# Optimization experiments

Hardware: AMD Instinct MI355X
Metric: run time of the kernel (lower is better)

Reference implementation:

```python
import jax, jax.numpy as jnp
import numpy as np

D = 256  # api_embed_channels
B = 8    # number of graphs
N = 128  # invoked APIs per graph (nodes); edges = N*N (fully connected incl. self-loops)
V = 10000


def setup_inputs() -> dict:
    key = jax.random.key(0)
    ks = jax.random.split(key, 12)
    s = 0.02
    return {
        "Xs": jax.random.normal(ks[0], (B, D), jnp.float32),
        "api_embeds": jax.random.normal(ks[1], (V, D), jnp.float32),
        "W1": jax.random.normal(ks[2], (2 * D, D), jnp.float32) * s,
        "b1": jnp.zeros((D,), jnp.float32),
        "W2": jax.random.normal(ks[3], (2 * D, D), jnp.float32) * s,
        "b2": jnp.zeros((D,), jnp.float32),
        "W3": jax.random.normal(ks[4], (2 * D, D), jnp.float32) * s,
        "b3": jnp.zeros((D,), jnp.float32),
        "W4": jax.random.normal(ks[5], (2 * D, 1), jnp.float32) * s,
        "b4": jnp.zeros((1,), jnp.float32),
        "invoked": jax.random.randint(ks[6], (B, N), 0, V, jnp.int32),
    }


def reference(Xs, api_embeds, W1, b1, W2, b2, W3, b3, W4, b4, invoked):
    # Gather invoked-API node features per graph: [B, N, D]
    feat = api_embeds[invoked]
    # Fully connected edge list in DGL insertion order: edge i -> (u=i//N, v=i%N).
    # src feats vary along axis 1 (u), dst feats along axis 2 (v).
    src = jnp.broadcast_to(feat[:, :, None, :], (B, N, N, D))
    dst = jnp.broadcast_to(feat[:, None, :, :], (B, N, N, D))
    # n2v_mlp1 per edge: Linear(2D -> D) on cat([src, dst])
    m = jnp.concatenate([src, dst], axis=-1) @ W1 + b1          # [B, N, N, D]
    # mean aggregation over incoming edges of dst v == mean over u (axis 1)
    e2n1 = jnp.mean(m, axis=1)                                   # [B, N, D]
    # n2n_mlp2: Linear(2D -> D) on cat([feat, e2n1])
    h = jnp.concatenate([feat, e2n1], axis=-1) @ W2 + b2         # [B, N, D]
    # n2v_mlp3 per edge: Linear(2D -> D) on cat([h_src, h_dst])
    hs = jnp.broadcast_to(h[:, :, None, :], (B, N, N, D))
    hd = jnp.broadcast_to(h[:, None, :, :], (B, N, N, D))
    ef = jnp.concatenate([hs, hd], axis=-1) @ W3 + b3            # [B, N, N, D]
    ef = ef.reshape(B, N * N, D)                                 # edge order u*N + v
    # edge_exist_mlp on cat([ef, x repeated per edge]): Linear(2D -> 1) + sigmoid
    x = jnp.broadcast_to(Xs[:, None, :], (B, N * N, D))
    logits = jnp.concatenate([ef, x], axis=-1) @ W4 + b4         # [B, N*N, 1]
    return jax.nn.sigmoid(logits)
```

## Files before the change

### kernel.cpp

```cpp
#include <hip/hip_runtime.h>


__device__ __forceinline__ float wred(float v) {
#pragma unroll
  for (int o = 32; o > 0; o >>= 1) v += __shfl_xor(v, o, 64);
  return v;
}
__device__ __forceinline__ float dot4(float4 a, float4 b) {
  return a.x * b.x + a.y * b.y + a.z * b.z + a.w * b.w;
}

#define OFF_PM   0
#define OFF_WA   131328
#define OFF_WB   131584
#define OFF_VA   131840
#define OFF_VB   132096
#define OFF_QS   132352
#define OFF_C0   132608
#define OFF_CALL 132616
#define OFF_FEAT 132624
#define WS_FLOATS_STAGED (OFF_FEAT + 262144)

__global__ __launch_bounds__(256) void k1(
    const float* __restrict__ Xs, const float* __restrict__ api,
    const float* __restrict__ W1, const float* __restrict__ b1,
    const float* __restrict__ W2, const float* __restrict__ b2,
    const float* __restrict__ W3, const float* __restrict__ b3,
    const float* __restrict__ W4, const float* __restrict__ b4,
    const int* __restrict__ invoked, float* __restrict__ ws) {
  const int blk = blockIdx.x, tid = threadIdx.x;
  float* PM = ws + OFF_PM;
  const float* W2bot = W2 + 256 * 256;
  __shared__ float w1s[2][256];
  __shared__ float4 part[2][4][64];

  if (blk < 256) {
    const int r0 = blk * 2;
    const int c4 = tid & 63, wv = tid >> 6;
    ((float*)w1s)[tid]       = W1[(size_t)r0 * 256 + tid];
    ((float*)w1s)[tid + 256] = W1[(size_t)r0 * 256 + 256 + tid];
    __syncthreads();
    const float4* w2b4 = (const float4*)W2bot;
    float4 a0 = make_float4(0.f, 0.f, 0.f, 0.f);
    float4 a1 = make_float4(0.f, 0.f, 0.f, 0.f);
    const int kb = wv * 64;
#pragma unroll 8
    for (int i = 0; i < 64; ++i) {
      int k = kb + i;
      float4 w = w2b4[k * 64 + c4];
      float x0 = w1s[0][k], x1 = w1s[1][k];
      a0.x += x0 * w.x; a0.y += x0 * w.y; a0.z += x0 * w.z; a0.w += x0 * w.w;
      a1.x += x1 * w.x; a1.y += x1 * w.y; a1.z += x1 * w.z; a1.w += x1 * w.w;
    }
    part[0][wv][c4] = a0;
    part[1][wv][c4] = a1;
    __syncthreads();
    if (tid < 128) {
      int row = tid >> 6, c = tid & 63;
      float4 p0 = part[row][0][c], p1 = part[row][1][c];
      float4 p2 = part[row][2][c], p3 = part[row][3][c];
      float4 s = make_float4(p0.x + p1.x + p2.x + p3.x,
                             p0.y + p1.y + p2.y + p3.y,
                             p0.z + p1.z + p2.z + p3.z,
                             p0.w + p1.w + p2.w + p3.w);
      int r = r0 + row;
      if (r >= 256) {
        float4 t = ((const float4*)(W2 + (size_t)(r - 256) * 256))[c];
        s.x += t.x; s.y += t.y; s.z += t.z; s.w += t.w;
      }
      ((float4*)(PM + (size_t)r * 256))[c] = s;
    }
  } else if (blk < 384) {
    const int lane = tid & 63, wv = tid >> 6;
    const int t = (blk - 256) * 4 + wv;
    float4 w4a = ((const float4*)W4)[lane];
    float4 rv = ((const float4*)(W3 + (size_t)t * 256))[lane];
    float s = wred(dot4(rv, w4a));
    if (lane == 0) {
      if (t < 256) ws[OFF_WA + t] = s; else ws[OFF_WB + t - 256] = s;
    }
  } else if (blk == 384) {
    const int lane = tid & 63, wv = tid >> 6;
    float4 w4a = ((const float4*)W4)[lane];
    float4 w4b4 = ((const float4*)W4)[lane + 64];
    float sb3 = wred(dot4(((const float4*)b3)[lane], w4a));
    for (int bi = wv; bi < 8; bi += 4) {
      float xd = wred(dot4(((const float4*)(Xs + (size_t)bi * 256))[lane], w4b4));
      if (lane == 0) ws[OFF_C0 + bi] = b4[0] + sb3 + xd;
    }
    const int c4 = tid & 63, rg = tid >> 6;
    const float4* w2b4 = (const float4*)W2bot;
    float4 acc = make_float4(0.f, 0.f, 0.f, 0.f);
#pragma unroll 8
    for (int i = 0; i < 64; ++i) {
      int k = rg * 64 + i;
      float4 w = w2b4[k * 64 + c4];
      float bv = b1[k];
      acc.x += bv * w.x; acc.y += bv * w.y; acc.z += bv * w.z; acc.w += bv * w.w;
    }
    part[0][rg][c4] = acc;
    __syncthreads();
    if (tid < 64) {
      float4 p0 = part[0][0][tid], p1 = part[0][1][tid];
      float4 p2 = part[0][2][tid], p3 = part[0][3][tid];
      float4 bb = ((const float4*)b2)[tid];
      float4 s = make_float4(p0.x + p1.x + p2.x + p3.x + bb.x,
                             p0.y + p1.y + p2.y + p3.y + bb.y,
                             p0.z + p1.z + p2.z + p3.z + bb.z,
                             p0.w + p1.w + p2.w + p3.w + bb.w);
      ((float4*)(PM + (size_t)512 * 256))[tid] = s;
    }
  } else {
    const int lane = tid & 63, wv = tid >> 6;
    const int row = (blk - 385) * 4 + wv;
    int idx = invoked[row];
    ((float4*)(ws + OFF_FEAT + (size_t)row * 256))[lane] =
        ((const float4*)(api + (size_t)idx * 256))[lane];
  }
}

__global__ __launch_bounds__(256) void k2(float* __restrict__ ws) {
  const int blk = blockIdx.x, tid = threadIdx.x;
  const int lane = tid & 63, wv = tid >> 6;
  const float* PM = ws + OFF_PM;
  float4 wa4 = ((const float4*)(ws + OFF_WA))[lane];
  float4 wb4 = ((const float4*)(ws + OFF_WB))[lane];
  if (blk < 128) {
    const int t = blk * 4 + wv;
    if (t < 256) {
      float4 rv = ((const float4*)(PM + (size_t)(256 + t) * 256))[lane];
      float sa = wred(dot4(rv, wa4));
      float sb = wred(dot4(rv, wb4));
      if (lane == 0) { ws[OFF_VA + t] = sa; ws[OFF_VB + t] = sb; }
    } else {
      float4 rv = ((const float4*)(PM + (size_t)(t - 256) * 256))[lane];
      float4 s4 = make_float4(wa4.x + wb4.x, wa4.y + wb4.y,
                              wa4.z + wb4.z, wa4.w + wb4.w);
      float s = wred(dot4(rv, s4));
      if (lane == 0) ws[OFF_QS + t - 256] = s;
    }
  } else {
    __shared__ float sAllSh;
    if (wv == 0) {
      float4 rv = ((const float4*)(PM + (size_t)512 * 256))[lane];
      float4 s4 = make_float4(wa4.x + wb4.x, wa4.y + wb4.y,
                              wa4.z + wb4.z, wa4.w + wb4.w);
      float s = wred(dot4(rv, s4));
      if (lane == 0) sAllSh = s;
    }
    __syncthreads();
    if (tid < 8) ws[OFF_CALL + tid] = ws[OFF_C0 + tid] + sAllSh;
  }
}

__global__ __launch_bounds__(1024) void k3(
    const float* __restrict__ api, const int* __restrict__ invoked,
    const float* __restrict__ ws, float* __restrict__ out, int staged) {
  const int g = blockIdx.x, tid = threadIdx.x;
  const int lane = tid & 63, wv = tid >> 6;
  __shared__ float Ash[128], Bsh[128], scsh[128];
  __shared__ float CbSh;

  float4 f[8];
  const int ub = wv * 8;
  if (staged) {
    const float4* fp =
        (const float4*)(ws + OFF_FEAT + (size_t)((g << 7) + ub) * 256);
#pragma unroll
    for (int i = 0; i < 8; ++i) f[i] = fp[(size_t)i * 64 + lane];
  } else {
    int idx[8];
#pragma unroll
    for (int i = 0; i < 8; ++i) idx[i] = invoked[(g << 7) + ub + i];
#pragma unroll
    for (int i = 0; i < 8; ++i)
      f[i] = ((const float4*)(api + (size_t)idx[i] * 256))[lane];
  }

  float4 va4 = ((const float4*)(ws + OFF_VA))[lane];
  float4 vb4 = ((const float4*)(ws + OFF_VB))[lane];
  float4 q4  = ((const float4*)(ws + OFF_QS))[lane];
#pragma unroll
  for (int i = 0; i < 8; ++i) {
    float sa = wred(dot4(f[i], va4));
    float sb = wred(dot4(f[i], vb4));
    float sc = wred(dot4(f[i], q4));
    if (lane == 0) { Ash[ub + i] = sa; Bsh[ub + i] = sb; scsh[ub + i] = sc; }
  }
  __syncthreads();
  if (wv == 0) {
    float t = scsh[lane] + scsh[lane + 64];
    t = wred(t);
    if (lane == 0) CbSh = t * (1.f / 128.f) + ws[OFF_CALL + g];
  }
  __syncthreads();
  const float Cb = CbSh;
  float4* ob = (float4*)(out + (g << 14));
#pragma unroll
  for (int j = 0; j < 4; ++j) {
    int e4 = tid + (j << 10);
    float a = Ash[e4 >> 5] + Cb;
    float4 bv = ((const float4*)Bsh)[e4 & 31];
    float4 r;
    r.x = 1.f / (1.f + __expf(-(a + bv.x)));
    r.y = 1.f / (1.f + __expf(-(a + bv.y)));
    r.z = 1.f / (1.f + __expf(-(a + bv.z)));
    r.w = 1.f / (1.f + __expf(-(a + bv.w)));
    ob[e4] = r;
  }
}

extern "C" void kernel_launch(void* const* d_in, const int* in_sizes, int n_in,
                              void* d_out, int out_size, void* d_ws, size_t ws_size,
                              hipStream_t stream) {
  const float* Xs  = (const float*)d_in[0];
  const float* api = (const float*)d_in[1];
  const float* W1  = (const float*)d_in[2];
  const float* b1  = (const float*)d_in[3];
  const float* W2  = (const float*)d_in[4];
  const float* b2  = (const float*)d_in[5];
  const float* W3  = (const float*)d_in[6];
  const float* b3  = (const float*)d_in[7];
  const float* W4  = (const float*)d_in[8];
  const float* b4  = (const float*)d_in[9];
  const int* invoked = (const int*)d_in[10];
  float* out = (float*)d_out;
  float* ws = (float*)d_ws;

  const int staged = (ws_size >= (size_t)WS_FLOATS_STAGED * sizeof(float));
  hipLaunchKernelGGL(k1, dim3(staged ? 641 : 385), dim3(256), 0, stream,
                     Xs, api, W1, b1, W2, b2, W3, b3, W4, b4, invoked, ws);
  hipLaunchKernelGGL(k2, dim3(129), dim3(256), 0, stream, ws);
  hipLaunchKernelGGL(k3, dim3(8), dim3(1024), 0, stream,
                     api, invoked, ws, out, staged);
}
```

Before: 25.98 us.

## Widen W1·W2 row tiles, drop feature staging, split k3 across 64 blocks

k1 now has each block compute 8 rows of the W1·W2 product instead of 2, so each W2 load is reused across more rows and the grid is smaller. The separate feature-gather blocks and their workspace staging are removed, and k3 always gathers embeddings directly. k3 launches 8 blocks per graph, each writing 16 rows of output, which spreads the output store and sigmoid across more CUs. The cost is that every block recomputes the same per-graph dot products, so the gather work is repeated 8 times. The wider tile also holds more accumulators per thread in k1, which raises register pressure.

Measured after the change: 22.91 us (median of 2 runs). 11.8% less time.

```diff
diff --git a/kernel.cpp b/kernel.cpp
--- a/kernel.cpp
+++ b/kernel.cpp
@@ -18,45 +18,50 @@
 #define OFF_QS   132352
 #define OFF_C0   132608
 #define OFF_CALL 132616
-#define OFF_FEAT 132624
-#define WS_FLOATS_STAGED (OFF_FEAT + 262144)
 
 __global__ __launch_bounds__(256) void k1(
-    const float* __restrict__ Xs, const float* __restrict__ api,
+    const float* __restrict__ Xs,
     const float* __restrict__ W1, const float* __restrict__ b1,
     const float* __restrict__ W2, const float* __restrict__ b2,
     const float* __restrict__ W3, const float* __restrict__ b3,
     const float* __restrict__ W4, const float* __restrict__ b4,
-    const int* __restrict__ invoked, float* __restrict__ ws) {
+    float* __restrict__ ws) {
   const int blk = blockIdx.x, tid = threadIdx.x;
   float* PM = ws + OFF_PM;
   const float* W2bot = W2 + 256 * 256;
-  __shared__ float w1s[2][256];
-  __shared__ float4 part[2][4][64];
-
-  if (blk < 256) {
-    const int r0 = blk * 2;
+  __shared__ float w1s[8][256];
+  __shared__ float4 part[8][4][64];
+
+  if (blk < 64) {
+    const int r0 = blk * 8;
     const int c4 = tid & 63, wv = tid >> 6;
-    ((float*)w1s)[tid]       = W1[(size_t)r0 * 256 + tid];
-    ((float*)w1s)[tid + 256] = W1[(size_t)r0 * 256 + 256 + tid];
+#pragma unroll
+    for (int i = 0; i < 8; ++i)
+      ((float*)w1s)[i * 256 + tid] = W1[(size_t)r0 * 256 + i * 256 + tid];
     __syncthreads();
     const float4* w2b4 = (const float4*)W2bot;
-    float4 a0 = make_float4(0.f, 0.f, 0.f, 0.f);
-    float4 a1 = make_float4(0.f, 0.f, 0.f, 0.f);
+    float4 acc[8];
+#pragma unroll
+    for (int i = 0; i < 8; ++i) acc[i] = make_float4(0.f, 0.f, 0.f, 0.f);
     const int kb = wv * 64;
-#pragma unroll 8
+#pragma unroll 4
     for (int i = 0; i < 64; ++i) {
       int k = kb + i;
       float4 w = w2b4[k * 64 + c4];
-      float x0 = w1s[0][k], x1 = w1s[1][k];
-      a0.x += x0 * w.x; a0.y += x0 * w.y; a0.z += x0 * w.z; a0.w += x0 * w.w;
-      a1.x += x1 * w.x; a1.y += x1 * w.y; a1.z += x1 * w.z; a1.w += x1 * w.w;
-    }
-    part[0][wv][c4] = a0;
-    part[1][wv][c4] = a1;
-    __syncthreads();
-    if (tid < 128) {
-      int row = tid >> 6, c = tid & 63;
+#pragma unroll
+      for (int r = 0; r < 8; ++r) {
+        float x = w1s[r][k];
+        acc[r].x += x * w.x; acc[r].y += x * w.y;
+        acc[r].z += x * w.z; acc[r].w += x * w.w;
+      }
+    }
+#pragma unroll
+    for (int r = 0; r < 8; ++r) part[r][wv][c4] = acc[r];
+    __syncthreads();
+#pragma unroll
+    for (int j = 0; j < 2; ++j) {
+      int item = tid + j * 256;
+      int row = item >> 6, c = item & 63;
       float4 p0 = part[row][0][c], p1 = part[row][1][c];
       float4 p2 = part[row][2][c], p3 = part[row][3][c];
       float4 s = make_float4(p0.x + p1.x + p2.x + p3.x,
@@ -70,16 +75,16 @@
       }
       ((float4*)(PM + (size_t)r * 256))[c] = s;
     }
-  } else if (blk < 384) {
+  } else if (blk < 192) {
     const int lane = tid & 63, wv = tid >> 6;
-    const int t = (blk - 256) * 4 + wv;
+    const int t = (blk - 64) * 4 + wv;
     float4 w4a = ((const float4*)W4)[lane];
     float4 rv = ((const float4*)(W3 + (size_t)t * 256))[lane];
     float s = wred(dot4(rv, w4a));
     if (lane == 0) {
       if (t < 256) ws[OFF_WA + t] = s; else ws[OFF_WB + t - 256] = s;
     }
-  } else if (blk == 384) {
+  } else {
     const int lane = tid & 63, wv = tid >> 6;
     float4 w4a = ((const float4*)W4)[lane];
     float4 w4b4 = ((const float4*)W4)[lane + 64];
@@ -110,12 +115,6 @@
                              p0.w + p1.w + p2.w + p3.w + bb.w);
       ((float4*)(PM + (size_t)512 * 256))[tid] = s;
     }
-  } else {
-    const int lane = tid & 63, wv = tid >> 6;
-    const int row = (blk - 385) * 4 + wv;
-    int idx = invoked[row];
-    ((float4*)(ws + OFF_FEAT + (size_t)row * 256))[lane] =
-        ((const float4*)(api + (size_t)idx * 256))[lane];
   }
 }
 
@@ -155,27 +154,21 @@
 
 __global__ __launch_bounds__(1024) void k3(
     const float* __restrict__ api, const int* __restrict__ invoked,
-    const float* __restrict__ ws, float* __restrict__ out, int staged) {
-  const int g = blockIdx.x, tid = threadIdx.x;
+    const float* __restrict__ ws, float* __restrict__ out) {
+  const int g = blockIdx.x >> 3, sub = blockIdx.x & 7;
+  const int tid = threadIdx.x;
   const int lane = tid & 63, wv = tid >> 6;
-  __shared__ float Ash[128], Bsh[128], scsh[128];
+  __shared__ alignas(16) float Ash[128], Bsh[128], scsh[128];
   __shared__ float CbSh;
 
   float4 f[8];
   const int ub = wv * 8;
-  if (staged) {
-    const float4* fp =
-        (const float4*)(ws + OFF_FEAT + (size_t)((g << 7) + ub) * 256);
-#pragma unroll
-    for (int i = 0; i < 8; ++i) f[i] = fp[(size_t)i * 64 + lane];
-  } else {
-    int idx[8];
-#pragma unroll
-    for (int i = 0; i < 8; ++i) idx[i] = invoked[(g << 7) + ub + i];
-#pragma unroll
-    for (int i = 0; i < 8; ++i)
-      f[i] = ((const float4*)(api + (size_t)idx[i] * 256))[lane];
-  }
+  int idx[8];
+#pragma unroll
+  for (int i = 0; i < 8; ++i) idx[i] = invoked[(g << 7) + ub + i];
+#pragma unroll
+  for (int i = 0; i < 8; ++i)
+    f[i] = ((const float4*)(api + (size_t)idx[i] * 256))[lane];
 
   float4 va4 = ((const float4*)(ws + OFF_VA))[lane];
   float4 vb4 = ((const float4*)(ws + OFF_VB))[lane];
@@ -195,18 +188,17 @@
   }
   __syncthreads();
   const float Cb = CbSh;
-  float4* ob = (float4*)(out + (g << 14));
-#pragma unroll
-  for (int j = 0; j < 4; ++j) {
-    int e4 = tid + (j << 10);
-    float a = Ash[e4 >> 5] + Cb;
-    float4 bv = ((const float4*)Bsh)[e4 & 31];
+  if (tid < 512) {
+    int u = (sub << 4) + (tid >> 5);
+    int v4 = tid & 31;
+    float a = Ash[u] + Cb;
+    float4 bv = ((const float4*)Bsh)[v4];
     float4 r;
     r.x = 1.f / (1.f + __expf(-(a + bv.x)));
     r.y = 1.f / (1.f + __expf(-(a + bv.y)));
     r.z = 1.f / (1.f + __expf(-(a + bv.z)));
     r.w = 1.f / (1.f + __expf(-(a + bv.w)));
-    ob[e4] = r;
+    ((float4*)(out + (g << 14) + (u << 7)))[v4] = r;
   }
 }
 
@@ -227,10 +219,9 @@
   float* out = (float*)d_out;
   float* ws = (float*)d_ws;
 
-  const int staged = (ws_size >= (size_t)WS_FLOATS_STAGED * sizeof(float));
-  hipLaunchKernelGGL(k1, dim3(staged ? 641 : 385), dim3(256), 0, stream,
-                     Xs, api, W1, b1, W2, b2, W3, b3, W4, b4, invoked, ws);
+  hipLaunchKernelGGL(k1, dim3(193), dim3(256), 0, stream,
+                     Xs, W1, b1, W2, b2, W3, b3, W4, b4, ws);
   hipLaunchKernelGGL(k2, dim3(129), dim3(256), 0, stream, ws);
-  hipLaunchKernelGGL(k3, dim3(8), dim3(1024), 0, stream,
-                     api, invoked, ws, out, staged);
-}
+  hipLaunchKernelGGL(k3, dim3(64), dim3(1024), 0, stream,
+                     api, invoked, ws, out);
+}
```
